# Performance work log

Hardware: AMD Instinct MI355X
Metric: run time of the kernel (lower is better)

Reference implementation:

```python
import math
import jax, jax.numpy as jnp
import numpy as np

B, C, T = 2, 512, 2048
HEADS, NFREQS, NDECAY = 8, 4, 4
HD = C // HEADS  # head dim = 64


def _conv1x1(x, W, b):
    # pointwise Conv1d: W [out, in], b [out], x [B, in, T]
    return jnp.einsum('oi,bit->bot', W, x) + b[:, None]


def setup_inputs() -> dict:
    key = jax.random.key(0)
    ks = jax.random.split(key, 12)
    s = 1.0 / math.sqrt(C)
    inp = {
        'x': jax.random.normal(ks[0], (B, C, T), jnp.float32),
        'Wq': jax.random.normal(ks[1], (C, C), jnp.float32) * s,
        'bq': jnp.zeros((C,), jnp.float32),
        'Wk': jax.random.normal(ks[2], (C, C), jnp.float32) * s,
        'bk': jnp.zeros((C,), jnp.float32),
        'Wc': jax.random.normal(ks[3], (C, C), jnp.float32) * s,
        'bc': jnp.zeros((C,), jnp.float32),
        'Wqf': jax.random.normal(ks[4], (HEADS * NFREQS, C), jnp.float32) * s,
        'bqf': jnp.zeros((HEADS * NFREQS,), jnp.float32),
        # query_decay init: weight *= 0.01, bias = -2 (as in the torch module)
        'Wqd': jax.random.normal(ks[5], (HEADS * NDECAY, C), jnp.float32) * (s * 0.01),
        'bqd': jnp.full((HEADS * NDECAY,), -2.0, jnp.float32),
        'Wp': jax.random.normal(ks[6], (C, C), jnp.float32) * s,
        'bp': jnp.zeros((C,), jnp.float32),
    }
    return inp


def reference(x, Wq, bq, Wk, bk, Wc, bc, Wqf, bqf, Wqd, bqd, Wp, bp):
    Bx, Cx, Tx = x.shape
    idx = jnp.arange(Tx, dtype=x.dtype)
    delta = idx[:, None] - idx[None, :]  # [T, T]

    queries = _conv1x1(x, Wq, bq).reshape(Bx, HEADS, HD, Tx)
    keys = _conv1x1(x, Wk, bk).reshape(Bx, HEADS, HD, Tx)
    dots = jnp.einsum('bhct,bhcs->bhts', keys, queries) / math.sqrt(HD)

    # frequency bias
    periods = jnp.arange(1, NFREQS + 1, dtype=x.dtype)
    freq_kernel = jnp.cos(2 * math.pi * delta / periods[:, None, None])  # [f, T, T]
    freq_q = _conv1x1(x, Wqf, bqf).reshape(Bx, HEADS, NFREQS, Tx) / math.sqrt(NFREQS)
    dots = dots + jnp.einsum('fts,bhfs->bhts', freq_kernel, freq_q)

    # decay bias
    decays = jnp.arange(1, NDECAY + 1, dtype=x.dtype)
    decay_q = jax.nn.sigmoid(_conv1x1(x, Wqd, bqd).reshape(Bx, HEADS, NDECAY, Tx)) / 2
    decay_kernel = -decays[:, None, None] * jnp.abs(delta) / math.sqrt(NDECAY)
    dots = dots + jnp.einsum('fts,bhfs->bhts', decay_kernel, decay_q)

    # mask self-attention diagonal with -100, softmax over keys axis (t, dim=2)
    eye = jnp.eye(Tx, dtype=bool)
    dots = jnp.where(eye[None, None], jnp.asarray(-100.0, x.dtype), dots)
    weights = jax.nn.softmax(dots, axis=2)

    content = _conv1x1(x, Wc, bc).reshape(Bx, HEADS, HD, Tx)
    result = jnp.einsum('bhts,bhct->bhcs', weights, content).reshape(Bx, Cx, Tx)
    return x + _conv1x1(result, Wp, bp)
```

## Files before the change

kernel.cpp:

```cpp
#include <hip/hip_runtime.h>
#include <math.h>

#define T_SEQ 2048
#define C_DIM 512
#define B_SZ  2
#define NHEAD 8
#define HD    64
#define DP    128
#define MTOT  1600
#define NTILE 32

typedef unsigned short u16t;
typedef unsigned int   u32t;
typedef float f32x4 __attribute__((ext_vector_type(4)));
typedef short s16x8 __attribute__((ext_vector_type(8)));

__device__ __forceinline__ u32t pack2(float a, float b) {
    u32t r;
    asm("v_cvt_pk_bf16_f32 %0, %1, %2" : "=v"(r) : "v"(a), "v"(b));
    return r;
}
__device__ __forceinline__ u16t f2bf(float f) {
    union { float f; u32t u; } v; v.f = f;
    u32t r = v.u + 0x7fffu + ((v.u >> 16) & 1u);
    return (u16t)(r >> 16);
}
__device__ __forceinline__ float bf2f(u16t h) {
    union { u32t u; float f; } v; v.u = (u32t)h << 16; return v.f;
}

#define GLD16(g, l) __builtin_amdgcn_global_load_lds( \
    (const __attribute__((address_space(1))) u32t*)(g), \
    (__attribute__((address_space(3))) u32t*)(l), 16, 0, 0)

__global__ __launch_bounds__(256)
void prep_kernel(const float* __restrict__ x, u16t* __restrict__ xT,
                 const float* __restrict__ Wq, const float* __restrict__ Wk,
                 const float* __restrict__ Wc, const float* __restrict__ Wqf,
                 const float* __restrict__ Wqd, const float* __restrict__ Wp,
                 const float* __restrict__ bq, const float* __restrict__ bk,
                 const float* __restrict__ bc, const float* __restrict__ bqf,
                 const float* __restrict__ bqd,
                 u16t* __restrict__ Wcat, u16t* __restrict__ Wpbf,
                 float* __restrict__ biascat)
{
    __shared__ float tile[64][65];
    int blk = blockIdx.x, tid = threadIdx.x;
    if (blk < 512) {
        int b = blk >> 8, rem = blk & 255;
        int c0 = (rem >> 5) << 6, t0 = (rem & 31) << 6;
        const float* xb = x + ((long long)b * C_DIM + c0) * T_SEQ + t0;
#pragma unroll
        for (int rr = 0; rr < 16; ++rr) {
            int row = rr * 4 + (tid >> 6);
            tile[row][tid & 63] = xb[(long long)row * T_SEQ + (tid & 63)];
        }
        __syncthreads();
        int tt = tid >> 2, cs = (tid & 3) * 16;
        u32t ov[8];
#pragma unroll
        for (int u = 0; u < 8; ++u)
            ov[u] = pack2(tile[cs + u * 2][tt], tile[cs + u * 2 + 1][tt]);
        u16t* dst = xT + ((long long)b * T_SEQ + t0 + tt) * C_DIM + c0 + cs;
        *(uint4*)(dst) = make_uint4(ov[0], ov[1], ov[2], ov[3]);
        *(uint4*)(dst + 8) = make_uint4(ov[4], ov[5], ov[6], ov[7]);
        return;
    }
    int r = blk - 512;
    if (r < MTOT) {
        const float* src;
        if (r < 512) src = Wq + (long long)r * C_DIM;
        else if (r < 1024) src = Wk + (long long)(r - 512) * C_DIM;
        else if (r < 1536) src = Wc + (long long)(r - 1024) * C_DIM;
        else if (r < 1568) src = Wqf + (long long)(r - 1536) * C_DIM;
        else src = Wqd + (long long)(r - 1568) * C_DIM;
        float2 v = *(const float2*)(src + tid * 2);
        *(u32t*)(Wcat + (long long)r * C_DIM + tid * 2) = pack2(v.x, v.y);
    } else if (r < MTOT + 512) {
        int rr = r - MTOT;
        float2 v = *(const float2*)(Wp + (long long)rr * C_DIM + tid * 2);
        *(u32t*)(Wpbf + (long long)rr * C_DIM + tid * 2) = pack2(v.x, v.y);
    } else {
        for (int i = tid; i < MTOT; i += 256) {
            float bv;
            if (i < 512) bv = bq[i];
            else if (i < 1024) bv = bk[i - 512];
            else if (i < 1536) bv = bc[i - 1024];
            else if (i < 1568) bv = bqf[i - 1536];
            else bv = bqd[i - 1568];
            biascat[i] = bv;
        }
    }
}

__global__ __launch_bounds__(256)
void gemm_kernel(const u16t* __restrict__ A, const u16t* __restrict__ Bm,
                 const float* __restrict__ biasv, const float* __restrict__ x,
                 u16t* __restrict__ Qbf, u16t* __restrict__ Kbf,
                 u16t* __restrict__ Vbf, float* __restrict__ fqd,
                 float* __restrict__ outp, int mode)
{
    __shared__ u16t At[2][64 * 64];
    __shared__ u16t Bt[2][64 * 64];
    int b = blockIdx.z, m0 = blockIdx.y * 64, n0 = blockIdx.x * 64;
    int tid = threadIdx.x, w = tid >> 6, lane = tid & 63;
    int l16 = lane & 15, l4 = lane >> 4;
    const u16t* Bb = Bm + (long long)b * T_SEQ * C_DIM;

    auto stage = [&](int kt, int bufi) {
        int k0 = kt * 64;
        const u16t* srcb = (w < 2) ? A + (long long)m0 * C_DIM + k0
                                   : Bb + (long long)n0 * C_DIM + k0;
        u16t* dstb = (w < 2) ? &At[bufi][0] : &Bt[bufi][0];
#pragma unroll
        for (int i = 0; i < 4; ++i) {
            int rb = (w & 1) * 32 + i * 8;
            int row = rb + (lane >> 3);
            int c = (lane & 7) ^ (row & 7);
            GLD16(srcb + (long long)row * C_DIM + c * 8, dstb + rb * 64);
        }
    };

    f32x4 acc[4] = {};
    stage(0, 0);
    for (int kt = 0; kt < 8; ++kt) {
        __syncthreads();
        if (kt < 7) stage(kt + 1, (kt + 1) & 1);
        const u16t* Bb2 = Bt[kt & 1];
        int nl = w * 16 + l16;
#pragma unroll
        for (int kb = 0; kb < 2; ++kb) {
            s16x8 bf = *(const s16x8*)(&Bb2[nl * 64 + (((kb * 4 + l4) ^ (l16 & 7)) * 8)]);
#pragma unroll
            for (int rt = 0; rt < 4; ++rt) {
                s16x8 af = *(const s16x8*)(&At[kt & 1][(rt * 16 + l16) * 64 + (((kb * 4 + l4) ^ (l16 & 7)) * 8)]);
                acc[rt] = __builtin_amdgcn_mfma_f32_16x16x32_bf16(af, bf, acc[rt], 0, 0, 0);
            }
        }
    }

    int n = n0 + w * 16 + l16;
    if (mode == 0) {
        if (m0 < 1024) {
            bool isQ = m0 < 512;
            int h = (isQ ? m0 : m0 - 512) >> 6;
            u16t* dst = (isQ ? Qbf : Kbf) + ((long long)(b * NHEAD + h) * T_SEQ + n) * DP;
            float sc = isQ ? 0.125f : 1.0f;
#pragma unroll
            for (int rt = 0; rt < 4; ++rt) {
                int d0 = (rt * 16 + l4 * 4) & 63;
                int m = m0 + rt * 16 + l4 * 4;
                float v0 = sc * (acc[rt][0] + biasv[m + 0]);
                float v1 = sc * (acc[rt][1] + biasv[m + 1]);
                float v2 = sc * (acc[rt][2] + biasv[m + 2]);
                float v3 = sc * (acc[rt][3] + biasv[m + 3]);
                *(uint2*)(dst + d0) = make_uint2(pack2(v0, v1), pack2(v2, v3));
            }
        } else if (m0 < 1536) {
#pragma unroll
            for (int rt = 0; rt < 4; ++rt)
#pragma unroll
                for (int j = 0; j < 4; ++j) {
                    int m = m0 + rt * 16 + l4 * 4 + j;
                    int c = m - 1024;
                    Vbf[((long long)b * C_DIM + c) * T_SEQ + n] = f2bf(acc[rt][j] + biasv[m]);
                }
        } else {
#pragma unroll
            for (int rt = 0; rt < 4; ++rt)
#pragma unroll
                for (int j = 0; j < 4; ++j) {
                    int m = m0 + rt * 16 + l4 * 4 + j;
                    fqd[((long long)b * 64 + (m - 1536)) * T_SEQ + n] = acc[rt][j] + biasv[m];
                }
        }
    } else {
#pragma unroll
        for (int rt = 0; rt < 4; ++rt)
#pragma unroll
            for (int j = 0; j < 4; ++j) {
                int m = m0 + rt * 16 + l4 * 4 + j;
                long long o = ((long long)b * C_DIM + m) * T_SEQ + n;
                outp[o] = acc[rt][j] + biasv[m] + x[o];
            }
    }
}

__global__ __launch_bounds__(256)
void ext_kernel(const float* __restrict__ fqd, u16t* __restrict__ Qbf,
                u16t* __restrict__ Kbf, float* __restrict__ dcoef,
                float* __restrict__ knorm)
{
    int s = blockIdx.x * 256 + threadIdx.x;
    int bh = blockIdx.y, b = bh >> 3, h = bh & 7;
    const float* base = fqd + (long long)b * 64 * T_SEQ;
    float dsum = 0.f;
    u32t eq[4], ek[4];
#pragma unroll
    for (int f = 0; f < 4; ++f) {
        float fq = base[(long long)(h * 4 + f) * T_SEQ + s] * 0.5f;
        float zd = base[(long long)(32 + h * 4 + f) * T_SEQ + s];
        dsum += (float)(f + 1) / (1.f + __expf(-zd));
        float a = 2.0f * (float)s / (float)(f + 1);
        float cv = cospif(a), sv = sinpif(a);
        ek[f] = pack2(cv, sv);
        eq[f] = pack2(fq * cv, fq * sv);
    }
    uint4 z = make_uint4(0, 0, 0, 0);
    u16t* qrow = Qbf + ((long long)bh * T_SEQ + s) * DP;
    *(uint4*)(qrow + 64) = make_uint4(eq[0], eq[1], eq[2], eq[3]);
#pragma unroll
    for (int i = 0; i < 7; ++i) *(uint4*)(qrow + 72 + i * 8) = z;
    u16t* krow = Kbf + ((long long)bh * T_SEQ + s) * DP;
    *(uint4*)(krow + 64) = make_uint4(ek[0], ek[1], ek[2], ek[3]);
#pragma unroll
    for (int i = 0; i < 7; ++i) *(uint4*)(krow + 72 + i * 8) = z;
    dcoef[(long long)bh * T_SEQ + s] = 0.25f * dsum;

    float ss = 0.f;
#pragma unroll
    for (int i = 0; i < 8; ++i) {
        s16x8 v = *(const s16x8*)(krow + i * 8);
#pragma unroll
        for (int e = 0; e < 8; ++e) { float f = bf2f((u16t)v[e]); ss += f * f; }
    }
    float nrm = sqrtf(ss + 4.1f);
#pragma unroll
    for (int off = 1; off < 64; off <<= 1)
        nrm = fmaxf(nrm, __shfl_xor(nrm, off, 64));
    if ((threadIdx.x & 63) == 0)
        knorm[bh * NTILE + (s >> 6)] = nrm;
}

__global__ __launch_bounds__(256)
void attn_kernel(const u16t* __restrict__ Qbf, const u16t* __restrict__ Kbf,
                 const u16t* __restrict__ Vbf, const float* __restrict__ dcoef,
                 const float* __restrict__ knorm, u16t* __restrict__ Rt)
{
    __shared__ u16t Kt[2][64 * DP];
    __shared__ u16t Vt[2][64 * 64];
    __shared__ u16t Pl[4][16 * 64];
    __shared__ u32t voteLds[4];

    int bh = blockIdx.y, b = bh >> 3, h = bh & 7;
    int j0 = blockIdx.x;
    int s0 = j0 * 64;
    int tid = threadIdx.x, w = tid >> 6, lane = tid & 63;
    int l16 = lane & 15, l4 = lane >> 4;
    const u16t* Qg = Qbf + (long long)bh * T_SEQ * DP;
    const u16t* Kg = Kbf + (long long)bh * T_SEQ * DP;
    const u16t* Vg = Vbf + ((long long)b * C_DIM + h * HD) * T_SEQ;
    int sl = w * 16 + l16;
    int sg = s0 + sl;

    s16x8 qf[3];
#pragma unroll
    for (int kb = 0; kb < 3; ++kb)
        qf[kb] = *(const s16x8*)(Qg + (long long)sg * DP + kb * 32 + l4 * 8);
    float qn2 = 0.f;
#pragma unroll
    for (int kb = 0; kb < 3; ++kb)
#pragma unroll
        for (int e = 0; e < 8; ++e) { float f = bf2f((u16t)qf[kb][e]); qn2 += f * f; }
    qn2 += __shfl_xor(qn2, 16, 64);
    qn2 += __shfl_xor(qn2, 32, 64);
    float qn = sqrtf(qn2);
    float dc = dcoef[(long long)bh * T_SEQ + sg];
    float mrun = -1e30f, lrun = 0.f;
    f32x4 O4[4] = {};

    auto stageKV = [&](int tt0, int bufi) {
#pragma unroll
        for (int i = 0; i < 4; ++i) {
            int rb = w * 16 + i * 4;
            int row = rb + (lane >> 4);
            int c = (lane & 15) ^ (row & 7);
            GLD16(Kg + (long long)(tt0 + row) * DP + c * 8, &Kt[bufi][rb * DP]);
        }
#pragma unroll
        for (int i = 0; i < 2; ++i) {
            int cb = w * 16 + i * 8;
            int cc = cb + (lane >> 3);
            int tc = (lane & 7) ^ (cc & 7);
            GLD16(Vg + (long long)cc * T_SEQ + tt0 + tc * 8, &Vt[bufi][cb * 64]);
        }
    };

    auto compute_tile = [&](int tj, int bufi, bool diag) {
        const u16t* Kb = Kt[bufi];
        const u16t* Vb = Vt[bufi];
        int t0 = tj * 64;
        f32x4 sacc[4] = {};
#pragma unroll
        for (int kb = 0; kb < 3; ++kb)
#pragma unroll
            for (int rt = 0; rt < 4; ++rt) {
                s16x8 af = *(const s16x8*)(&Kb[(rt * 16 + l16) * DP + (((kb * 4 + l4) ^ (l16 & 7)) * 8)]);
                sacc[rt] = __builtin_amdgcn_mfma_f32_16x16x32_bf16(af, qf[kb], sacc[rt], 0, 0, 0);
            }
        float cm = mrun;
        float pv[4][4];
#pragma unroll
        for (int rt = 0; rt < 4; ++rt) {
            int tb = t0 + rt * 16 + l4 * 4;
#pragma unroll
            for (int j = 0; j < 4; ++j) {
                int t = tb + j;
                float v = sacc[rt][j] - fabsf((float)(t - sg)) * dc;
                if (diag && t == sg) v = -100.f;
                pv[rt][j] = v;
                cm = fmaxf(cm, v);
            }
        }
        cm = fmaxf(cm, __shfl_xor(cm, 16, 64));
        cm = fmaxf(cm, __shfl_xor(cm, 32, 64));
        if (__any(cm > mrun)) {
            float scale = __expf(mrun - cm);
            mrun = cm;
            lrun *= scale;
#pragma unroll
            for (int rt = 0; rt < 4; ++rt) O4[rt] *= scale;
        }
        float psum = 0.f;
#pragma unroll
        for (int rt = 0; rt < 4; ++rt)
#pragma unroll
            for (int j = 0; j < 4; ++j) {
                float p = __expf(pv[rt][j] - mrun);
                pv[rt][j] = p;
                psum += p;
            }
        psum += __shfl_xor(psum, 16, 64);
        psum += __shfl_xor(psum, 32, 64);
        lrun += psum;
#pragma unroll
        for (int rt = 0; rt < 4; ++rt) {
            int tl = rt * 16 + l4 * 4;
            int cp = (tl >> 3) ^ (l16 & 7);
            *(uint2*)(&Pl[w][l16 * 64 + cp * 8 + (tl & 7)]) =
                make_uint2(pack2(pv[rt][0], pv[rt][1]), pack2(pv[rt][2], pv[rt][3]));
        }
#pragma unroll
        for (int kb = 0; kb < 2; ++kb) {
            s16x8 pf = *(const s16x8*)(&Pl[w][l16 * 64 + (((kb * 4 + l4) ^ (l16 & 7)) * 8)]);
#pragma unroll
            for (int rt = 0; rt < 4; ++rt) {
                s16x8 vf = *(const s16x8*)(&Vb[(rt * 16 + l16) * 64 + (((kb * 4 + l4) ^ (l16 & 7)) * 8)]);
                O4[rt] = __builtin_amdgcn_mfma_f32_16x16x32_bf16(vf, pf, O4[rt], 0, 0, 0);
            }
        }
    };

    int seq[3]; int ns = 0;
    seq[ns++] = j0;
    if (j0 + 1 < NTILE) seq[ns++] = j0 + 1;
    if (j0 > 0) seq[ns++] = j0 - 1;
    stageKV(seq[0] * 64, 0);
    for (int i = 0; i < ns; ++i) {
        __syncthreads();
        if (i + 1 < ns) stageKV(seq[i + 1] * 64, (i + 1) & 1);
        compute_tile(seq[i], i & 1, seq[i] == j0);
    }

    u32t mask = 0;
    const float* knb = knorm + bh * NTILE;
    for (int j = 0; j < NTILE; ++j) {
        int d = j > j0 ? j - j0 : j0 - j;
        if (d <= 1) continue;
        float minD = (float)((d - 1) * 64 + 1);
        float bound = qn * knb[j] - dc * minD;
        if (__any(bound > mrun - 15.f)) mask |= 1u << j;
    }
    voteLds[w] = mask;
    __syncthreads();
    mask = voteLds[0] | voteLds[1] | voteLds[2] | voteLds[3];

    int parity = ns & 1;
    u32t rem = mask;
    if (rem) {
        int j = (int)__builtin_ctz(rem);
        stageKV(j * 64, parity);
        while (true) {
            rem &= rem - 1;
            __syncthreads();
            int nj = rem ? (int)__builtin_ctz(rem) : -1;
            if (nj >= 0) stageKV(nj * 64, parity ^ 1);
            compute_tile(j, parity, false);
            if (nj < 0) break;
            parity ^= 1;
            j = nj;
        }
    }

    __syncthreads();
    float inv = 1.f / lrun;
#pragma unroll
    for (int rt = 0; rt < 4; ++rt) {
        O4[rt] *= inv;
        int cb = rt * 16 + l4 * 4;
        int cp = (cb >> 3) ^ (sl & 7);
        *(uint2*)(&Kt[0][sl * 64 + cp * 8 + (cb & 7)]) =
            make_uint2(pack2(O4[rt][0], O4[rt][1]), pack2(O4[rt][2], O4[rt][3]));
    }
    __syncthreads();
    {
        int row = tid >> 2;
        int rsw = row & 7;
        u16t* dst = Rt + ((long long)b * T_SEQ + s0 + row) * C_DIM + h * HD;
#pragma unroll
        for (int i = 0; i < 2; ++i) {
            int cc = (tid & 3) + i * 4;
            uint4 v = *(const uint4*)(&Kt[0][row * 64 + ((cc ^ rsw) * 8)]);
            *(uint4*)(dst + cc * 8) = v;
        }
    }
}

extern "C" void kernel_launch(void* const* d_in, const int* in_sizes, int n_in,
                              void* d_out, int out_size, void* d_ws, size_t ws_size,
                              hipStream_t stream)
{
    const float* x   = (const float*)d_in[0];
    const float* Wq  = (const float*)d_in[1];
    const float* bq  = (const float*)d_in[2];
    const float* Wk  = (const float*)d_in[3];
    const float* bk  = (const float*)d_in[4];
    const float* Wc  = (const float*)d_in[5];
    const float* bc  = (const float*)d_in[6];
    const float* Wqf = (const float*)d_in[7];
    const float* bqf = (const float*)d_in[8];
    const float* Wqd = (const float*)d_in[9];
    const float* bqd = (const float*)d_in[10];
    const float* Wp  = (const float*)d_in[11];
    const float* bp  = (const float*)d_in[12];
    float* out = (float*)d_out;

    char* p = (char*)d_ws;
    u16t* Wcat = (u16t*)p;    p += (long long)MTOT * C_DIM * 2;
    u16t* Wpbf = (u16t*)p;    p += (long long)C_DIM * C_DIM * 2;
    float* biascat = (float*)p; p += MTOT * 4;
    u16t* xT = (u16t*)p;      p += (long long)B_SZ * T_SEQ * C_DIM * 2;
    u16t* Qbf = (u16t*)p;     p += (long long)16 * T_SEQ * DP * 2;
    u16t* Kbf = (u16t*)p;     p += (long long)16 * T_SEQ * DP * 2;
    u16t* Vbf = (u16t*)p;     p += (long long)B_SZ * C_DIM * T_SEQ * 2;
    float* fqd = (float*)p;   p += (long long)B_SZ * 64 * T_SEQ * 4;
    float* dcoef = (float*)p; p += (long long)16 * T_SEQ * 4;
    float* knorm = (float*)p; p += (long long)16 * NTILE * 4;
    u16t* Rt = (u16t*)p;      p += (long long)B_SZ * T_SEQ * C_DIM * 2;

    dim3 blk(256);
    hipLaunchKernelGGL(prep_kernel, dim3(512 + MTOT + 512 + 1), blk, 0, stream,
                       x, xT, Wq, Wk, Wc, Wqf, Wqd, Wp, bq, bk, bc, bqf, bqd,
                       Wcat, Wpbf, biascat);
    hipLaunchKernelGGL(gemm_kernel, dim3(T_SEQ / 64, MTOT / 64, B_SZ), blk, 0, stream,
                       Wcat, xT, biascat, nullptr, Qbf, Kbf, Vbf, fqd, nullptr, 0);
    hipLaunchKernelGGL(ext_kernel, dim3(T_SEQ / 256, 16), blk, 0, stream,
                       fqd, Qbf, Kbf, dcoef, knorm);
    hipLaunchKernelGGL(attn_kernel, dim3(T_SEQ / 64, 16), blk, 0, stream,
                       Qbf, Kbf, Vbf, dcoef, knorm, Rt);
    hipLaunchKernelGGL(gemm_kernel, dim3(T_SEQ / 64, C_DIM / 64, B_SZ), blk, 0, stream,
                       Wpbf, Rt, bp, x, nullptr, nullptr, nullptr, nullptr, out, 1);
}
```

Before: 59.16 us.

## Split attention into single-wave blocks reading K/V directly from global memory

```diff
diff --git a/kernel.cpp b/kernel.cpp
--- a/kernel.cpp
+++ b/kernel.cpp
@@ -232,26 +232,22 @@
         knorm[bh * NTILE + (s >> 6)] = nrm;
 }
 
-__global__ __launch_bounds__(256)
+__global__ __launch_bounds__(64)
 void attn_kernel(const u16t* __restrict__ Qbf, const u16t* __restrict__ Kbf,
                  const u16t* __restrict__ Vbf, const float* __restrict__ dcoef,
                  const float* __restrict__ knorm, u16t* __restrict__ Rt)
 {
-    __shared__ u16t Kt[2][64 * DP];
-    __shared__ u16t Vt[2][64 * 64];
-    __shared__ u16t Pl[4][16 * 64];
-    __shared__ u32t voteLds[4];
+    __shared__ u16t Pl[16 * 64];
 
     int bh = blockIdx.y, b = bh >> 3, h = bh & 7;
-    int j0 = blockIdx.x;
-    int s0 = j0 * 64;
-    int tid = threadIdx.x, w = tid >> 6, lane = tid & 63;
+    int s0 = blockIdx.x * 16;
+    int j0 = s0 >> 6;
+    int lane = threadIdx.x;
     int l16 = lane & 15, l4 = lane >> 4;
     const u16t* Qg = Qbf + (long long)bh * T_SEQ * DP;
     const u16t* Kg = Kbf + (long long)bh * T_SEQ * DP;
     const u16t* Vg = Vbf + ((long long)b * C_DIM + h * HD) * T_SEQ;
-    int sl = w * 16 + l16;
-    int sg = s0 + sl;
+    int sg = s0 + l16;
 
     s16x8 qf[3];
 #pragma unroll
@@ -269,33 +265,14 @@
     float mrun = -1e30f, lrun = 0.f;
     f32x4 O4[4] = {};
 
-    auto stageKV = [&](int tt0, int bufi) {
-#pragma unroll
-        for (int i = 0; i < 4; ++i) {
-            int rb = w * 16 + i * 4;
-            int row = rb + (lane >> 4);
-            int c = (lane & 15) ^ (row & 7);
-            GLD16(Kg + (long long)(tt0 + row) * DP + c * 8, &Kt[bufi][rb * DP]);
-        }
-#pragma unroll
-        for (int i = 0; i < 2; ++i) {
-            int cb = w * 16 + i * 8;
-            int cc = cb + (lane >> 3);
-            int tc = (lane & 7) ^ (cc & 7);
-            GLD16(Vg + (long long)cc * T_SEQ + tt0 + tc * 8, &Vt[bufi][cb * 64]);
-        }
-    };
-
-    auto compute_tile = [&](int tj, int bufi, bool diag) {
-        const u16t* Kb = Kt[bufi];
-        const u16t* Vb = Vt[bufi];
+    auto compute_tile = [&](int tj) {
         int t0 = tj * 64;
         f32x4 sacc[4] = {};
 #pragma unroll
         for (int kb = 0; kb < 3; ++kb)
 #pragma unroll
             for (int rt = 0; rt < 4; ++rt) {
-                s16x8 af = *(const s16x8*)(&Kb[(rt * 16 + l16) * DP + (((kb * 4 + l4) ^ (l16 & 7)) * 8)]);
+                s16x8 af = *(const s16x8*)(Kg + (long long)(t0 + rt * 16 + l16) * DP + kb * 32 + l4 * 8);
                 sacc[rt] = __builtin_amdgcn_mfma_f32_16x16x32_bf16(af, qf[kb], sacc[rt], 0, 0, 0);
             }
         float cm = mrun;
@@ -307,7 +284,7 @@
             for (int j = 0; j < 4; ++j) {
                 int t = tb + j;
                 float v = sacc[rt][j] - fabsf((float)(t - sg)) * dc;
-                if (diag && t == sg) v = -100.f;
+                if (t == sg) v = -100.f;
                 pv[rt][j] = v;
                 cm = fmaxf(cm, v);
             }
@@ -333,86 +310,55 @@
         psum += __shfl_xor(psum, 16, 64);
         psum += __shfl_xor(psum, 32, 64);
         lrun += psum;
+        __syncthreads();
 #pragma unroll
         for (int rt = 0; rt < 4; ++rt) {
             int tl = rt * 16 + l4 * 4;
             int cp = (tl >> 3) ^ (l16 & 7);
-            *(uint2*)(&Pl[w][l16 * 64 + cp * 8 + (tl & 7)]) =
+            *(uint2*)(&Pl[l16 * 64 + cp * 8 + (tl & 7)]) =
                 make_uint2(pack2(pv[rt][0], pv[rt][1]), pack2(pv[rt][2], pv[rt][3]));
         }
+        __syncthreads();
 #pragma unroll
         for (int kb = 0; kb < 2; ++kb) {
-            s16x8 pf = *(const s16x8*)(&Pl[w][l16 * 64 + (((kb * 4 + l4) ^ (l16 & 7)) * 8)]);
+            s16x8 pf = *(const s16x8*)(&Pl[l16 * 64 + (((kb * 4 + l4) ^ (l16 & 7)) * 8)]);
 #pragma unroll
             for (int rt = 0; rt < 4; ++rt) {
-                s16x8 vf = *(const s16x8*)(&Vb[(rt * 16 + l16) * 64 + (((kb * 4 + l4) ^ (l16 & 7)) * 8)]);
+                s16x8 vf = *(const s16x8*)(Vg + (long long)(rt * 16 + l16) * T_SEQ + t0 + kb * 32 + l4 * 8);
                 O4[rt] = __builtin_amdgcn_mfma_f32_16x16x32_bf16(vf, pf, O4[rt], 0, 0, 0);
             }
         }
     };
 
-    int seq[3]; int ns = 0;
-    seq[ns++] = j0;
-    if (j0 + 1 < NTILE) seq[ns++] = j0 + 1;
-    if (j0 > 0) seq[ns++] = j0 - 1;
-    stageKV(seq[0] * 64, 0);
-    for (int i = 0; i < ns; ++i) {
-        __syncthreads();
-        if (i + 1 < ns) stageKV(seq[i + 1] * 64, (i + 1) & 1);
-        compute_tile(seq[i], i & 1, seq[i] == j0);
-    }
+    compute_tile(j0);
+    if (j0 + 1 < NTILE) compute_tile(j0 + 1);
+    if (j0 > 0) compute_tile(j0 - 1);
 
     u32t mask = 0;
     const float* knb = knorm + bh * NTILE;
     for (int j = 0; j < NTILE; ++j) {
         int d = j > j0 ? j - j0 : j0 - j;
         if (d <= 1) continue;
-        float minD = (float)((d - 1) * 64 + 1);
+        float minD = (j > j0) ? (float)(j * 64 - (s0 + 15))
+                              : (float)(s0 - (j * 64 + 63));
         float bound = qn * knb[j] - dc * minD;
         if (__any(bound > mrun - 15.f)) mask |= 1u << j;
     }
-    voteLds[w] = mask;
-    __syncthreads();
-    mask = voteLds[0] | voteLds[1] | voteLds[2] | voteLds[3];
-
-    int parity = ns & 1;
+
     u32t rem = mask;
-    if (rem) {
+    while (rem) {
         int j = (int)__builtin_ctz(rem);
-        stageKV(j * 64, parity);
-        while (true) {
-            rem &= rem - 1;
-            __syncthreads();
-            int nj = rem ? (int)__builtin_ctz(rem) : -1;
-            if (nj >= 0) stageKV(nj * 64, parity ^ 1);
-            compute_tile(j, parity, false);
-            if (nj < 0) break;
-            parity ^= 1;
-            j = nj;
-        }
-    }
-
-    __syncthreads();
+        rem &= rem - 1;
+        compute_tile(j);
+    }
+
     float inv = 1.f / lrun;
+    u16t* dstRow = Rt + ((long long)b * T_SEQ + sg) * C_DIM + h * HD;
 #pragma unroll
     for (int rt = 0; rt < 4; ++rt) {
         O4[rt] *= inv;
-        int cb = rt * 16 + l4 * 4;
-        int cp = (cb >> 3) ^ (sl & 7);
-        *(uint2*)(&Kt[0][sl * 64 + cp * 8 + (cb & 7)]) =
+        *(uint2*)(dstRow + rt * 16 + l4 * 4) =
             make_uint2(pack2(O4[rt][0], O4[rt][1]), pack2(O4[rt][2], O4[rt][3]));
-    }
-    __syncthreads();
-    {
-        int row = tid >> 2;
-        int rsw = row & 7;
-        u16t* dst = Rt + ((long long)b * T_SEQ + s0 + row) * C_DIM + h * HD;
-#pragma unroll
-        for (int i = 0; i < 2; ++i) {
-            int cc = (tid & 3) + i * 4;
-            uint4 v = *(const uint4*)(&Kt[0][row * 64 + ((cc ^ rsw) * 8)]);
-            *(uint4*)(dst + cc * 8) = v;
-        }
     }
 }
 
@@ -456,7 +402,7 @@
                        Wcat, xT, biascat, nullptr, Qbf, Kbf, Vbf, fqd, nullptr, 0);
     hipLaunchKernelGGL(ext_kernel, dim3(T_SEQ / 256, 16), blk, 0, stream,
                        fqd, Qbf, Kbf, dcoef, knorm);
-    hipLaunchKernelGGL(attn_kernel, dim3(T_SEQ / 64, 16), blk, 0, stream,
+    hipLaunchKernelGGL(attn_kernel, dim3(T_SEQ / 16, 16), dim3(64), 0, stream,
                        Qbf, Kbf, Vbf, dcoef, knorm, Rt);
     hipLaunchKernelGGL(gemm_kernel, dim3(T_SEQ / 64, C_DIM / 64, B_SZ), blk, 0, stream,
                        Wpbf, Rt, bp, x, nullptr, nullptr, nullptr, nullptr, out, 1);
```

New measurement: 75.50 us. +27.6%, slower.
